# Kernel tuning notes

Hardware: AMD Instinct MI355X
Metric: run time of the kernel (lower is better)

The kernel has to match this reference:

```python
import jax, jax.numpy as jnp
import numpy as np

B, S, P, E, H = 2, 2048, 2048, 1024, 16
DH = E // H  # 64


def setup_inputs() -> dict:
    key = jax.random.key(0)
    ks = jax.random.split(key, 9)
    query = jax.random.normal(ks[0], (B, S, E), jnp.float32)
    key_in = jax.random.normal(ks[1], (B, S, E), jnp.float32)
    value = jax.random.normal(ks[2], (B, S, E), jnp.float32)
    past_k = jax.random.normal(ks[3], (B, H, P, DH), jnp.float32)
    past_v = jax.random.normal(ks[4], (B, H, P, DH), jnp.float32)
    # additive causal mask over the current block; all past positions visible
    i = jnp.arange(S)[:, None]          # query positions within current block
    j = jnp.arange(P + S)[None, :]      # absolute key positions
    causal = (j <= i + P)
    attn_mask = jnp.where(causal, 0.0, -1e9).astype(jnp.float32)[None, None]  # [1,1,S,P+S]
    sc = 1.0 / np.sqrt(E)
    Wq = jax.random.normal(ks[5], (E, E), jnp.float32) * sc
    Wk = jax.random.normal(ks[6], (E, E), jnp.float32) * sc
    Wv = jax.random.normal(ks[7], (E, E), jnp.float32) * sc
    Wo = jax.random.normal(ks[8], (E, E), jnp.float32) * sc
    return {"query": query, "key": key_in, "value": value,
            "past_k": past_k, "past_v": past_v, "attn_mask": attn_mask,
            "Wq": Wq, "Wk": Wk, "Wv": Wv, "Wo": Wo}


def _split_heads(x):
    # [B, S, E] -> [B, H, S, DH]  (matches view + transpose(1,2))
    b, s, _ = x.shape
    return x.reshape(b, s, H, DH).transpose(0, 2, 1, 3)


def reference(query, key, value, past_k, past_v, attn_mask, Wq, Wk, Wv, Wo):
    q = _split_heads(query @ Wq.T)          # [B,H,S,DH]
    k_new = _split_heads(key @ Wk.T)        # [B,H,S,DH]
    v_new = _split_heads(value @ Wv.T)      # [B,H,S,DH]
    k = jnp.concatenate([past_k, k_new], axis=2)   # [B,H,T,DH], T=P+S
    v = jnp.concatenate([past_v, v_new], axis=2)
    scores = jnp.einsum('bhse,bhte->bhst', q, k) / np.sqrt(DH)
    scores = scores + attn_mask
    attn = jax.nn.softmax(scores, axis=-1)
    out = jnp.einsum('bhst,bhtd->bshd', attn, v)    # [B,S,H,DH]
    out = out.reshape(query.shape[0], -1, E)         # [B,S,E]
    return out @ Wo.T
```

## Files before the change

### kernel.cpp

```cpp
#include <hip/hip_runtime.h>

#define BB 2
#define SS 2048
#define PP 2048
#define TT 4096
#define EE 1024
#define HH 16
#define DH 64

typedef __attribute__((ext_vector_type(8))) __bf16 bf16x8;
typedef __attribute__((ext_vector_type(4))) __bf16 bf16x4;
typedef __attribute__((ext_vector_type(4))) float f32x4;
typedef __attribute__((ext_vector_type(16))) float f32x16;

__device__ __forceinline__ void gload_lds16(const void* g, void* l) {
  __builtin_amdgcn_global_load_lds(
      (const __attribute__((address_space(1))) void*)g,
      (__attribute__((address_space(3))) void*)l, 16, 0, 0);
}

#define MFMA16(a, b, c) __builtin_amdgcn_mfma_f32_16x16x32_bf16((a), (b), (c), 0, 0, 0)
#define MFMA32(a, b, c) __builtin_amdgcn_mfma_f32_32x32x16_bf16((a), (b), (c), 0, 0, 0)

__device__ __forceinline__ unsigned cvtpk_bf16(float lo, float hi) {
  unsigned r;
  asm("v_cvt_pk_bf16_f32 %0, %1, %2" : "=v"(r) : "v"(lo), "v"(hi));
  return r;
}

struct ConvDesc {
  const float* s[8];
  __bf16* d[8];
  int n4[8];
};

__global__ __launch_bounds__(256) void convert_and_transpose(ConvDesc cd,
                                                             const float* __restrict__ pv,
                                                             __bf16* __restrict__ vt) {
  if (blockIdx.y < 8) {
    const int a = blockIdx.y;
    const float* __restrict__ src = cd.s[a];
    __bf16* __restrict__ dst = cd.d[a];
    const int n4 = cd.n4[a];
    const int stride = gridDim.x * blockDim.x;
    for (int i = blockIdx.x * blockDim.x + threadIdx.x; i < n4; i += stride) {
      float4 v = ((const float4*)src)[i];
      bf16x4 o = {(__bf16)v.x, (__bf16)v.y, (__bf16)v.z, (__bf16)v.w};
      ((bf16x4*)dst)[i] = o;
    }
  } else {
    __shared__ float tile[64][65];
    const int bh = blockIdx.x >> 5;
    const int k0 = (blockIdx.x & 31) * 64;
    const int tx = threadIdx.x & 63, ty = threadIdx.x >> 6;
#pragma unroll
    for (int i = 0; i < 16; ++i) {
      const int r = ty + i * 4;
      tile[r][tx] = pv[((size_t)bh * PP + k0 + r) * DH + tx];
    }
    __syncthreads();
#pragma unroll
    for (int i = 0; i < 16; ++i) {
      const int d = ty + i * 4;
      vt[((size_t)bh * DH + d) * TT + k0 + tx] = (__bf16)tile[tx][d];
    }
  }
}

__device__ __forceinline__ void gemm_core(const __bf16* A, const __bf16* Bt, __bf16* As,
                                          __bf16* Bs, int m0, int n0, f32x4 acc[4][4]) {
  const int tid = threadIdx.x, w = tid >> 6, lane = tid & 63;
  const int l15 = lane & 15, lg = lane >> 4;
  const int wr = w >> 1, wc = w & 1;
  const int cidx = w * 128 + lane;
  const int r0 = cidx >> 2, c0 = cidx & 3;
  const int r1 = r0 + 16;
  for (int kt = 0; kt < 32; ++kt) {
    const int k0 = kt * 32;
    if (kt) __syncthreads();
    gload_lds16(A + (size_t)(m0 + r0) * EE + k0 + c0 * 8, As + w * 1024);
    gload_lds16(A + (size_t)(m0 + r1) * EE + k0 + c0 * 8, As + w * 1024 + 512);
    gload_lds16(Bt + (size_t)(n0 + r0) * EE + k0 + c0 * 8, Bs + w * 1024);
    gload_lds16(Bt + (size_t)(n0 + r1) * EE + k0 + c0 * 8, Bs + w * 1024 + 512);
    __syncthreads();
    bf16x8 af[4], bf[4];
#pragma unroll
    for (int mi = 0; mi < 4; ++mi)
      af[mi] = *(const bf16x8*)&As[(wr * 64 + mi * 16 + l15) * 32 + lg * 8];
#pragma unroll
    for (int ni = 0; ni < 4; ++ni)
      bf[ni] = *(const bf16x8*)&Bs[(wc * 64 + ni * 16 + l15) * 32 + lg * 8];
#pragma unroll
    for (int mi = 0; mi < 4; ++mi)
#pragma unroll
      for (int ni = 0; ni < 4; ++ni) acc[mi][ni] = MFMA16(af[mi], bf[ni], acc[mi][ni]);
  }
}

__global__ __launch_bounds__(512, 2) void proj_qkv256(
    const __bf16* __restrict__ xq, const __bf16* __restrict__ xk, const __bf16* __restrict__ xv,
    const __bf16* __restrict__ wqb, const __bf16* __restrict__ wkb, const __bf16* __restrict__ wvb,
    __bf16* __restrict__ qws, __bf16* __restrict__ kproj, __bf16* __restrict__ vt) {
  __shared__ alignas(16) __bf16 As[2][16384];
  __shared__ alignas(16) __bf16 Bs[2][16384];

  const int tid = threadIdx.x;
  const int w = tid >> 6, lane = tid & 63;
  const int l15 = lane & 15, lg = (lane >> 4) & 3;
  const int wm = w >> 2, wn = w & 3;

  const int z = blockIdx.z;
  const __bf16* A = (z == 0) ? xq : (z == 1) ? xk : xv;
  const __bf16* Bt = (z == 0) ? wqb : (z == 1) ? wkb : wvb;
  const int m0 = blockIdx.y * 256, n0 = blockIdx.x * 256;

  f32x4 acc[8][4];
  const f32x4 fz = {0.f, 0.f, 0.f, 0.f};
#pragma unroll
  for (int mf = 0; mf < 8; ++mf)
#pragma unroll
    for (int nf = 0; nf < 4; ++nf) acc[mf][nf] = fz;

  const int srow = lane >> 3;
  const int scg = (lane & 7) ^ srow;
  const __bf16* baseA = A + (size_t)(m0 + w * 8 + srow) * EE + scg * 8;
  const __bf16* baseB = Bt + (size_t)(n0 + w * 8 + srow) * EE + scg * 8;

  const int rowA = wm * 128 + l15;
  const int rowB = wn * 64 + l15;
  const int swz = l15 & 7;
  const int aoff0 = (lg ^ swz) << 3;
  const int aoff1 = ((4 + lg) ^ swz) << 3;

#define STGH(BUF, BASE, HALF, KT)                                                         \
  {                                                                                       \
    gload_lds16((BASE) + (size_t)((HALF)*128) * EE + (size_t)(KT)*64,                     \
                &(BUF)[(((HALF)*128) + w * 8) * 64]);                                     \
    gload_lds16((BASE) + (size_t)((HALF)*128 + 64) * EE + (size_t)(KT)*64,                \
                &(BUF)[(((HALF)*128 + 64) + w * 8) * 64]);                                \
  }

#define LOADB(CUR)                                                                        \
  _Pragma("unroll") for (int nf = 0; nf < 4; ++nf) {                                      \
    bfr[2 * nf] = *(const bf16x8*)&Bs[CUR][(rowB + nf * 16) * 64 + aoff0];                \
    bfr[2 * nf + 1] = *(const bf16x8*)&Bs[CUR][(rowB + nf * 16) * 64 + aoff1];            \
  }

#define PHASE(CUR, MB, STAGECODE, VMCODE)                                                 \
  {                                                                                       \
    afr[0] = *(const bf16x8*)&As[CUR][(rowA + (MB)*16) * 64 + aoff0];                     \
    afr[1] = *(const bf16x8*)&As[CUR][(rowA + (MB)*16) * 64 + aoff1];                     \
    afr[2] = *(const bf16x8*)&As[CUR][(rowA + (MB)*16 + 16) * 64 + aoff0];                \
    afr[3] = *(const bf16x8*)&As[CUR][(rowA + (MB)*16 + 16) * 64 + aoff1];                \
    STAGECODE;                                                                            \
    __builtin_amdgcn_s_barrier();                                                         \
    __builtin_amdgcn_s_setprio(1);                                                        \
    _Pragma("unroll") for (int nf = 0; nf < 4; ++nf) {                                    \
      acc[MB][nf] = MFMA16(afr[0], bfr[2 * nf], acc[MB][nf]);                             \
      acc[MB][nf] = MFMA16(afr[1], bfr[2 * nf + 1], acc[MB][nf]);                         \
      acc[(MB) + 1][nf] = MFMA16(afr[2], bfr[2 * nf], acc[(MB) + 1][nf]);                 \
      acc[(MB) + 1][nf] = MFMA16(afr[3], bfr[2 * nf + 1], acc[(MB) + 1][nf]);             \
    }                                                                                     \
    __builtin_amdgcn_s_setprio(0);                                                        \
    VMCODE;                                                                               \
    __builtin_amdgcn_s_barrier();                                                         \
  }

  STGH(As[0], baseA, 0, 0);
  STGH(As[0], baseA, 1, 0);
  STGH(Bs[0], baseB, 0, 0);
  STGH(Bs[0], baseB, 1, 0);
  STGH(Bs[1], baseB, 0, 1);
  STGH(Bs[1], baseB, 1, 1);
  asm volatile("s_waitcnt vmcnt(4)" ::: "memory");
  __builtin_amdgcn_s_barrier();

  for (int i = 0; i < 8; ++i) {
    const int kt1 = 2 * i + 1, kt2 = 2 * i + 2, kt3 = 2 * i + 3;
    const bool st = (i < 7);
    bf16x8 bfr[8], afr[4];
    LOADB(0);
    PHASE(0, 0, { STGH(As[1], baseA, 0, kt1); }, {});
    PHASE(0, 2, { STGH(As[1], baseA, 1, kt1); }, {});
    PHASE(0, 4, { if (st) STGH(Bs[0], baseB, 0, kt2); }, {});
    PHASE(0, 6, { if (st) STGH(Bs[0], baseB, 1, kt2); }, {
      if (st) { asm volatile("s_waitcnt vmcnt(4)" ::: "memory"); }
      else    { asm volatile("s_waitcnt vmcnt(0)" ::: "memory"); }
    });
    LOADB(1);
    PHASE(1, 0, { if (st) STGH(As[0], baseA, 0, kt2); }, {});
    PHASE(1, 2, { if (st) STGH(As[0], baseA, 1, kt2); }, {});
    PHASE(1, 4, { if (st) STGH(Bs[1], baseB, 0, kt3); }, {});
    PHASE(1, 6, { if (st) STGH(Bs[1], baseB, 1, kt3); }, {
      if (st) { asm volatile("s_waitcnt vmcnt(4)" ::: "memory"); }
      else    { asm volatile("s_waitcnt vmcnt(0)" ::: "memory"); }
    });
  }
#undef PHASE
#undef LOADB
#undef STGH

  if (z < 2) {
    __bf16* dst = (z == 0) ? qws : kproj;
    const float sc = (z == 0) ? 0.180336884f : 1.0f;
#pragma unroll
    for (int mf = 0; mf < 8; ++mf)
#pragma unroll
      for (int nf = 0; nf < 4; ++nf) {
        const int mb = m0 + wm * 128 + mf * 16 + lg * 4;
        const int n = n0 + wn * 64 + nf * 16 + l15;
#pragma unroll
        for (int r = 0; r < 4; ++r)
          dst[(size_t)(mb + r) * EE + n] = (__bf16)(acc[mf][nf][r] * sc);
      }
  } else {
#pragma unroll
    for (int mf = 0; mf < 8; ++mf)
#pragma unroll
      for (int nf = 0; nf < 4; ++nf) {
        const int mb = m0 + wm * 128 + mf * 16 + lg * 4;
        const int n = n0 + wn * 64 + nf * 16 + l15;
        const int bb = mb >> 11, s = mb & (SS - 1);
        const int hh = n >> 6, dd = n & 63;
        bf16x4 pk = {(__bf16)acc[mf][nf][0], (__bf16)acc[mf][nf][1], (__bf16)acc[mf][nf][2],
                     (__bf16)acc[mf][nf][3]};
        *(bf16x4*)&vt[((size_t)(bb * HH + hh) * DH + dd) * TT + PP + s] = pk;
      }
  }
}

__global__ __launch_bounds__(256) void gemm_out(const __bf16* __restrict__ A,
                                                const __bf16* __restrict__ Bt,
                                                float* __restrict__ C) {
  __shared__ alignas(16) __bf16 As[4096];
  __shared__ alignas(16) __bf16 Bs[4096];
  const int m0 = blockIdx.y * 128, n0 = blockIdx.x * 128;
  f32x4 acc[4][4];
  const f32x4 fz = {0.f, 0.f, 0.f, 0.f};
#pragma unroll
  for (int mi = 0; mi < 4; ++mi)
#pragma unroll
    for (int ni = 0; ni < 4; ++ni) acc[mi][ni] = fz;
  gemm_core(A, Bt, As, Bs, m0, n0, acc);

  const int tid = threadIdx.x, w = tid >> 6, lane = tid & 63;
  const int l15 = lane & 15, lg = lane >> 4;
  const int wr = w >> 1, wc = w & 1;
#pragma unroll
  for (int mi = 0; mi < 4; ++mi)
#pragma unroll
    for (int ni = 0; ni < 4; ++ni) {
      const int mb = m0 + wr * 64 + mi * 16 + lg * 4;
      const int n = n0 + wc * 64 + ni * 16 + l15;
#pragma unroll
      for (int r = 0; r < 4; ++r) C[(size_t)(mb + r) * EE + n] = acc[mi][ni][r];
    }
}

__global__ __launch_bounds__(512) void attn_kernel(const __bf16* __restrict__ q_ws,
                                                   const __bf16* __restrict__ kpast,
                                                   const __bf16* __restrict__ kproj,
                                                   const __bf16* __restrict__ vt,
                                                   __bf16* __restrict__ o0,
                                                   __bf16* __restrict__ o1,
                                                   float2* __restrict__ stats) {
  __shared__ alignas(16) __bf16 lds[3][2][4096];

  const int tid = threadIdx.x;
  const int w = tid >> 6, lane = tid & 63;
  const int l31 = lane & 31, hi = lane >> 5, l7 = lane & 7;

  const int bh = blockIdx.y;
  const int half = blockIdx.z;
  const int qb2 = half ? (7 - blockIdx.x) : blockIdx.x;
  const int b = bh >> 4, h = bh & 15;
  const int i0 = qb2 * 256;
  const int qw0 = i0 + w * 32;

  const int nt = 4 * qb2 + 36;
  const int tstart = half ? (nt >> 1) : 0;
  const int tend = half ? nt : (nt >> 1);

  const float NEGM = -12.0f;

  bf16x8 qf[4];
  {
    const __bf16* qbase = q_ws + (size_t)(b * SS + qw0 + l31) * EE + h * DH + hi * 8;
#pragma unroll
    for (int c = 0; c < 4; ++c) qf[c] = *(const bf16x8*)(qbase + 16 * c);
  }

  f32x16 oacc[2];
#pragma unroll
  for (int r = 0; r < 16; ++r) {
    oacc[0][r] = 0.f;
    oacc[1][r] = 0.f;
  }
  float l_run = 0.f;

  const int srow = tid >> 3;
  const int scg = (tid & 7) ^ (srow & 7);

  const __bf16* kp = kpast + ((size_t)bh * PP + tstart * 64 + srow) * DH + scg * 8;
  const __bf16* kn =
      kproj + (ptrdiff_t)(b * SS - PP + tstart * 64 + srow) * EE + h * DH + scg * 8;
  const __bf16* vp = vt + ((size_t)bh * DH + srow) * TT + tstart * 64 + scg * 8;

#define STAGE(buf, T)                                  \
  {                                                    \
    gload_lds16(((T) < 32) ? kp : kn, &lds[buf][0][w * 512]); \
    gload_lds16(vp, &lds[buf][1][w * 512]);            \
    kp += 64 * DH;                                     \
    kn += (ptrdiff_t)64 * EE;                          \
    vp += 64;                                          \
  }

#define ITER(T, CUR, NXT)                                                                \
  {                                                                                      \
    if ((T) + 1 < tend) {                                                                \
      asm volatile("s_waitcnt vmcnt(2)" ::: "memory");        \
    } else {                                                                             \
      asm volatile("s_waitcnt vmcnt(0)" ::: "memory");        \
    }                                                                                    \
    __builtin_amdgcn_s_barrier();  \
    if ((T) + 2 < tend) STAGE(NXT, (T) + 2);                                             \
    const int kv0 = (T)*64;                                                              \
    if (kv0 <= qw0 + 31 + PP) {                             \
      f32x16 p[2];                                                                       \
      _Pragma("unroll") for (int s = 0; s < 2; ++s)                                      \
      _Pragma("unroll") for (int r = 0; r < 16; ++r) p[s][r] = NEGM;                     \
      const __bf16* Kb = lds[CUR][0];                                                    \
      __builtin_amdgcn_s_setprio(1);                                                     \
      _Pragma("unroll") for (int s = 0; s < 2; ++s)                                      \
      _Pragma("unroll") for (int c = 0; c < 4; ++c) {                                    \
        const bf16x8 kf =                                                                \
            *(const bf16x8*)&Kb[(32 * s + l31) * 64 + (((2 * c + hi) ^ l7) << 3)];       \
        p[s] = MFMA32(kf, qf[c], p[s]);                                                  \
      }                                                                                  \
      __builtin_amdgcn_s_setprio(0);                                                     \
      if (kv0 + 63 > qw0 + PP) {                                                         \
        const int qa = qw0 + l31 + PP;                                                   \
        _Pragma("unroll") for (int s = 0; s < 2; ++s)                                    \
        _Pragma("unroll") for (int r = 0; r < 16; ++r) {                                 \
          const int key = kv0 + 32 * s + (r & 3) + 8 * (r >> 2) + 4 * hi;                \
          if (key > qa) p[s][r] = -1e30f;                                                \
        }                                                                                \
      }                                                                                  \
      _Pragma("unroll") for (int s = 0; s < 2; ++s)                                      \
      _Pragma("unroll") for (int r = 0; r < 16; ++r)                                     \
          p[s][r] = __builtin_amdgcn_exp2f(p[s][r]);                                     \
      float s16[16];                                                                     \
      _Pragma("unroll") for (int r = 0; r < 16; ++r) s16[r] = p[0][r] + p[1][r];         \
      _Pragma("unroll") for (int st = 8; st > 0; st >>= 1)                               \
      _Pragma("unroll") for (int r = 0; r < st; ++r) s16[r] += s16[r + st];              \
      l_run += s16[0] + __shfl_xor(s16[0], 32, 64);                                      \
      bf16x8 pb[4];                                                                      \
      _Pragma("unroll") for (int s = 0; s < 2; ++s)                                      \
      _Pragma("unroll") for (int u = 0; u < 2; ++u) {                                    \
        unsigned a0 = cvtpk_bf16(p[s][8 * u + 0], p[s][8 * u + 1]);                      \
        unsigned a1 = cvtpk_bf16(p[s][8 * u + 2], p[s][8 * u + 3]);                      \
        unsigned b0 = cvtpk_bf16(p[s][8 * u + 4], p[s][8 * u + 5]);                      \
        unsigned b1 = cvtpk_bf16(p[s][8 * u + 6], p[s][8 * u + 7]);                      \
        asm volatile("v_permlane32_swap_b32 %0, %1" : "+v"(a0), "+v"(b0));               \
        asm volatile("v_permlane32_swap_b32 %0, %1" : "+v"(a1), "+v"(b1));               \
        union {                                                                          \
          unsigned u32[4];                                                               \
          bf16x8 v;                                                                      \
        } pk;                                                                            \
        pk.u32[0] = a0;                                                                  \
        pk.u32[1] = a1;                                                                  \
        pk.u32[2] = b0;                                                                  \
        pk.u32[3] = b1;                                                                  \
        pb[2 * s + u] = pk.v;                                                            \
      }                                                                                  \
      const __bf16* Vb = lds[CUR][1];                                                    \
      __builtin_amdgcn_s_setprio(1);                                                     \
      _Pragma("unroll") for (int u = 0; u < 4; ++u) {                                    \
        const bf16x8 vf0 = *(const bf16x8*)&Vb[l31 * 64 + (((2 * u + hi) ^ l7) << 3)];   \
        oacc[0] = MFMA32(vf0, pb[u], oacc[0]);                                           \
        const bf16x8 vf1 =                                                               \
            *(const bf16x8*)&Vb[(32 + l31) * 64 + (((2 * u + hi) ^ l7) << 3)];           \
        oacc[1] = MFMA32(vf1, pb[u], oacc[1]);                                           \
      }                                                                                  \
      __builtin_amdgcn_s_setprio(0);                                                     \
    }                                                                                    \
  }

  STAGE(0, tstart);
  if (tstart + 1 < tend) STAGE(1, tstart + 1);

  const int ntp = tend - tstart;
  int j = 0;
  for (; j + 3 <= ntp; j += 3) {
    ITER(tstart + j, 0, 2);
    ITER(tstart + j + 1, 1, 0);
    ITER(tstart + j + 2, 2, 1);
  }
  if (j < ntp) ITER(tstart + j, 0, 2);
  if (j + 1 < ntp) ITER(tstart + j + 1, 1, 0);

  const float inv = 1.0f / l_run;
  __bf16* od = half ? o1 : o0;
  const size_t orow = (size_t)(b * SS + qw0 + l31) * EE + h * DH;
#pragma unroll
  for (int dblk = 0; dblk < 2; ++dblk)
#pragma unroll
    for (int g = 0; g < 4; ++g) {
      bf16x4 v4;
#pragma unroll
      for (int r4 = 0; r4 < 4; ++r4) v4[r4] = (__bf16)(oacc[dblk][4 * g + r4] * inv);
      *(bf16x4*)&od[orow + 32 * dblk + 8 * g + 4 * hi] = v4;
    }
  if (hi == 0) {
    stats[((size_t)half * (BB * SS) + b * SS + qw0 + l31) * HH + h] = float2{12.0f, l_run};
  }
#undef ITER
#undef STAGE
}

__global__ __launch_bounds__(256) void combine_halves(const __bf16* __restrict__ o0,
                                                      const __bf16* __restrict__ o1,
                                                      const float2* __restrict__ st,
                                                      __bf16* __restrict__ ao) {
  const int tid = threadIdx.x;
  const int row = blockIdx.x * 2 + (tid >> 7);
  const int c8 = tid & 127;
  const int h = c8 >> 3;
  const float2 s0 = st[(size_t)row * HH + h];
  const float2 s1 = st[(size_t)(BB * SS + row) * HH + h];
  const float m = fmaxf(s0.x, s1.x);
  float w0 = __builtin_amdgcn_exp2f(s0.x - m) * s0.y;
  float w1 = __builtin_amdgcn_exp2f(s1.x - m) * s1.y;
  const float inv = 1.0f / (w0 + w1);
  w0 *= inv;
  w1 *= inv;
  const size_t off = (size_t)row * EE + c8 * 8;
  const bf16x8 a = *(const bf16x8*)(o0 + off);
  const bf16x8 b = *(const bf16x8*)(o1 + off);
  bf16x8 o;
#pragma unroll
  for (int r = 0; r < 8; ++r) o[r] = (__bf16)(w0 * (float)a[r] + w1 * (float)b[r]);
  *(bf16x8*)(ao + off) = o;
}

extern "C" void kernel_launch(void* const* d_in, const int* in_sizes, int n_in, void* d_out,
                              int out_size, void* d_ws, size_t ws_size, hipStream_t stream) {
  const float* query = (const float*)d_in[0];
  const float* key_in = (const float*)d_in[1];
  const float* value = (const float*)d_in[2];
  const float* past_k = (const float*)d_in[3];
  const float* past_v = (const float*)d_in[4];
  const float* Wq = (const float*)d_in[6];
  const float* Wk = (const float*)d_in[7];
  const float* Wv = (const float*)d_in[8];
  const float* Wo = (const float*)d_in[9];

  char* ws = (char*)d_ws;
  __bf16* XQ = (__bf16*)(ws + 0);
  __bf16* XK = (__bf16*)(ws + 8388608);
  __bf16* XV = (__bf16*)(ws + 16777216);
  __bf16* WQB = (__bf16*)(ws + 25165824);
  __bf16* WKB = (__bf16*)(ws + 27262976);
  __bf16* WVB = (__bf16*)(ws + 29360128);
  __bf16* WOB = (__bf16*)(ws + 31457280);
  __bf16* QW = (__bf16*)(ws + 33554432);
  __bf16* KP = (__bf16*)(ws + 41943040);
  __bf16* KN = (__bf16*)(ws + 50331648);
  __bf16* VT = (__bf16*)(ws + 58720256);
  float2* ST = (float2*)(ws + 0);
  __bf16* O1 = (__bf16*)(ws + 2097152);
  __bf16* O0 = (__bf16*)(ws + 75497472);
  __bf16* AO = QW;

  ConvDesc cd;
  cd.s[0] = query;  cd.d[0] = XQ;  cd.n4[0] = 1048576;
  cd.s[1] = key_in; cd.d[1] = XK;  cd.n4[1] = 1048576;
  cd.s[2] = value;  cd.d[2] = XV;  cd.n4[2] = 1048576;
  cd.s[3] = Wq;     cd.d[3] = WQB; cd.n4[3] = 262144;
  cd.s[4] = Wk;     cd.d[4] = WKB; cd.n4[4] = 262144;
  cd.s[5] = Wv;     cd.d[5] = WVB; cd.n4[5] = 262144;
  cd.s[6] = Wo;     cd.d[6] = WOB; cd.n4[6] = 262144;
  cd.s[7] = past_k; cd.d[7] = KP;  cd.n4[7] = 1048576;

  convert_and_transpose<<<dim3(1024, 9, 1), 256, 0, stream>>>(cd, past_v, VT);
  proj_qkv256<<<dim3(4, 16, 3), 512, 0, stream>>>(XQ, XK, XV, WQB, WKB, WVB, QW, KN, VT);
  attn_kernel<<<dim3(8, 32, 2), 512, 0, stream>>>(QW, KP, KN, VT, O0, O1, ST);
  combine_halves<<<dim3(2048, 1, 1), 256, 0, stream>>>(O0, O1, ST, AO);
  gemm_out<<<dim3(8, 32, 1), 256, 0, stream>>>(AO, WOB, (float*)d_out);
}
```

Measured before the change: 154.4 us.

## Deepen attention K/V pipeline to five LDS slots with one barrier per two tiles

The attention kernel's K/V staging grows from a triple-buffered ring to a five-slot LDS ring. Each barrier now covers two 64-key tiles, and two tiles are prefetched after it, so the kernel syncs half as often and has more loads in flight. In exchange, LDS use per block rises from 48 KB to 80 KB. That can cut the number of resident 512-thread blocks per CU and reduce latency hiding across blocks. The main loop is unrolled by ten tiles, with a pair-wise tail that relies on the per-half tile count always being even.

```diff
diff --git a/kernel.cpp b/kernel.cpp
--- a/kernel.cpp
+++ b/kernel.cpp
@@ -264,7 +264,7 @@
                                                    __bf16* __restrict__ o0,
                                                    __bf16* __restrict__ o1,
                                                    float2* __restrict__ stats) {
-  __shared__ alignas(16) __bf16 lds[3][2][4096];
+  __shared__ alignas(16) __bf16 lds[5][2][4096];
 
   const int tid = threadIdx.x;
   const int w = tid >> 6, lane = tid & 63;
@@ -315,21 +315,14 @@
     vp += 64;                                          \
   }
 
-#define ITER(T, CUR, NXT)                                                                \
+#define COMPUTE(T, SLOT)                                                                 \
   {                                                                                      \
-    if ((T) + 1 < tend) {                                                                \
-      asm volatile("s_waitcnt vmcnt(2)" ::: "memory");        \
-    } else {                                                                             \
-      asm volatile("s_waitcnt vmcnt(0)" ::: "memory");        \
-    }                                                                                    \
-    __builtin_amdgcn_s_barrier();  \
-    if ((T) + 2 < tend) STAGE(NXT, (T) + 2);                                             \
     const int kv0 = (T)*64;                                                              \
-    if (kv0 <= qw0 + 31 + PP) {                             \
+    if (kv0 <= qw0 + 31 + PP) {                                                          \
       f32x16 p[2];                                                                       \
       _Pragma("unroll") for (int s = 0; s < 2; ++s)                                      \
       _Pragma("unroll") for (int r = 0; r < 16; ++r) p[s][r] = NEGM;                     \
-      const __bf16* Kb = lds[CUR][0];                                                    \
+      const __bf16* Kb = lds[SLOT][0];                                                   \
       __builtin_amdgcn_s_setprio(1);                                                     \
       _Pragma("unroll") for (int s = 0; s < 2; ++s)                                      \
       _Pragma("unroll") for (int c = 0; c < 4; ++c) {                                    \
@@ -373,7 +366,7 @@
         pk.u32[3] = b1;                                                                  \
         pb[2 * s + u] = pk.v;                                                            \
       }                                                                                  \
-      const __bf16* Vb = lds[CUR][1];                                                    \
+      const __bf16* Vb = lds[SLOT][1];                                                   \
       __builtin_amdgcn_s_setprio(1);                                                     \
       _Pragma("unroll") for (int u = 0; u < 4; ++u) {                                    \
         const bf16x8 vf0 = *(const bf16x8*)&Vb[l31 * 64 + (((2 * u + hi) ^ l7) << 3)];   \
@@ -386,18 +379,41 @@
     }                                                                                    \
   }
 
+#define PAIR(T, SA, SB, S3, S4)                                                          \
+  {                                                                                      \
+    if ((T) + 2 < tend) {                                                                \
+      asm volatile("s_waitcnt vmcnt(2)" ::: "memory");    \
+    } else {                                                                             \
+      asm volatile("s_waitcnt vmcnt(0)" ::: "memory");                                   \
+    }                                                                                    \
+    __builtin_amdgcn_s_barrier();                                                        \
+    if ((T) + 3 < tend) STAGE(S3, (T) + 3);                                              \
+    if ((T) + 4 < tend) STAGE(S4, (T) + 4);                                              \
+    COMPUTE((T), SA);                                                                    \
+    COMPUTE((T) + 1, SB);                                                                \
+  }
+
   STAGE(0, tstart);
-  if (tstart + 1 < tend) STAGE(1, tstart + 1);
+  STAGE(1, tstart + 1);
+  STAGE(2, tstart + 2);
 
   const int ntp = tend - tstart;
   int j = 0;
-  for (; j + 3 <= ntp; j += 3) {
-    ITER(tstart + j, 0, 2);
-    ITER(tstart + j + 1, 1, 0);
-    ITER(tstart + j + 2, 2, 1);
-  }
-  if (j < ntp) ITER(tstart + j, 0, 2);
-  if (j + 1 < ntp) ITER(tstart + j + 1, 1, 0);
+  for (; j + 10 <= ntp; j += 10) {
+    const int t = tstart + j;
+    PAIR(t, 0, 1, 3, 4);
+    PAIR(t + 2, 2, 3, 0, 1);
+    PAIR(t + 4, 4, 0, 2, 3);
+    PAIR(t + 6, 1, 2, 4, 0);
+    PAIR(t + 8, 3, 4, 1, 2);
+  }
+  {
+    const int t = tstart + j;
+    if (j + 2 <= ntp) PAIR(t, 0, 1, 3, 4);
+    if (j + 4 <= ntp) PAIR(t + 2, 2, 3, 0, 1);
+    if (j + 6 <= ntp) PAIR(t + 4, 4, 0, 2, 3);
+    if (j + 8 <= ntp) PAIR(t + 6, 1, 2, 4, 0);
+  }
 
   const float inv = 1.0f / l_run;
   __bf16* od = half ? o1 : o0;
@@ -414,7 +430,8 @@
   if (hi == 0) {
     stats[((size_t)half * (BB * SS) + b * SS + qw0 + l31) * HH + h] = float2{12.0f, l_run};
   }
-#undef ITER
+#undef PAIR
+#undef COMPUTE
 #undef STAGE
 }
 
```

Measured after the change: 163.0 us. 1.06x slower.
